# Kernel optimization log

Measured on AMD Instinct MI355X. Metric: run time of the kernel, lower is better.

The kernel has to match this reference:

```python
import jax, jax.numpy as jnp
import numpy as np

H = 1024
W = 1024
N = 128
K1 = 21.7  # on-road exponential loss scale
K2 = 40.0  # off-road exponential loss scale


def setup_inputs() -> dict:
    key = jax.random.key(0)
    k1, k2 = jax.random.split(key)
    hd_map = (jax.random.uniform(k1, (H, W)) < 0.3).astype(jnp.float32)
    # integer pixel coordinates, kept away from the border so the 2x2
    # neighbor window is always in-bounds (matches typical usage)
    prediction = jax.random.randint(k2, (N, 2), 2, H - 2).astype(jnp.int32)
    return {"hd_map": hd_map, "prediction": prediction}


def reference(hd_map, prediction):
    Hm, Wm = hd_map.shape
    p = prediction.astype(jnp.float32)  # [N,2]

    # Separable squared distances from each point to every pixel.
    # NOTE: faithful to the original, nonzero()[:,0] (row) is compared with
    # point[0] and nonzero()[:,1] (col) with point[1].
    rows = jnp.arange(Hm, dtype=jnp.float32)
    cols = jnp.arange(Wm, dtype=jnp.float32)
    dr2 = (rows[None, :] - p[:, 0:1]) ** 2  # [N,H]
    dc2 = (cols[None, :] - p[:, 1:2]) ** 2  # [N,W]
    d2 = dr2[:, :, None] + dc2[:, None, :]  # [N,H,W]

    INF = jnp.float32(1e30)
    on_mask = hd_map != 0  # nonzero pixels of hd_map (non-drivable)
    # min squared distance to nearest nonzero pixel of hd_map
    d2_on = jnp.min(jnp.where(on_mask[None], d2, INF), axis=(1, 2))  # [N]
    # min squared distance to nearest nonzero pixel of (1 - hd_map)
    d2_off = jnp.min(jnp.where(on_mask[None], INF, d2), axis=(1, 2))  # [N]

    px = prediction[:, 0]
    py = prediction[:, 1]
    # is_outside_frame: point[0] vs shape[0], point[1] vs shape[1] (faithful)
    outside_frame = (px < 0) | (px > Hm) | (py < 0) | (py > Wm)

    # is_outside_road: 2x2 window im[py-1:py+1, px-1:px+1] contains a 1
    ir = jnp.stack([py - 1, py - 1, py, py], axis=-1)  # [N,4]
    ic = jnp.stack([px - 1, px, px - 1, px], axis=-1)  # [N,4]
    neigh = hd_map[ir, ic]  # [N,4]
    outside_road = jnp.any(neigh == 1.0, axis=-1)

    ln2 = jnp.log(jnp.float32(2.0))
    # off-road: exp(d * ln(2)/k2); on-road: exp(-d^2 / k1)
    loss_off = jnp.exp(jnp.sqrt(d2_off) * (ln2 / K2))
    loss_on = jnp.exp(-d2_on / K1)

    per_point = jnp.where(
        outside_frame,
        jnp.float32(0.0),
        jnp.where(outside_road, loss_off, loss_on),
    )
    return jnp.mean(per_point)
```

## Files before the change

kernel.cpp:

```cpp
#include <hip/hip_runtime.h>
#include <math.h>

#define HMAP 1024
#define WMAP 1024

__device__ __forceinline__ int clampi(int x, int hi) {
    return x < 0 ? 0 : (x > hi ? hi : x);
}

__global__ __launch_bounds__(64)
void roadloss_points(const float* __restrict__ hd_map,
                     const int* __restrict__ pred,
                     int n,
                     float* __restrict__ ws) {
    const int pt   = blockIdx.x;
    const int lane = threadIdx.x;
    if (pt >= n) return;

    const int px = pred[2 * pt];
    const int py = pred[2 * pt + 1];

    const int r0c = clampi(py - 1, HMAP - 1), r1c = clampi(py, HMAP - 1);
    const int c0c = clampi(px - 1, WMAP - 1), c1c = clampi(px, WMAP - 1);
    const float n00 = hd_map[r0c * WMAP + c0c];
    const float n01 = hd_map[r0c * WMAP + c1c];
    const float n10 = hd_map[r1c * WMAP + c0c];
    const float n11 = hd_map[r1c * WMAP + c1c];

    const int R = 16;

    float v[18];
#pragma unroll
    for (int ii = 0; ii < 18; ++ii) {
        int i  = lane + ii * 64;
        int dr = i / 33 - R;
        int dc = i % 33 - R;
        int r  = clampi(px + dr, HMAP - 1);
        int c  = clampi(py + dc, WMAP - 1);
        v[ii]  = hd_map[r * WMAP + c];
    }

    float on0 = 1e30f, off0 = 1e30f, on1 = 1e30f, off1 = 1e30f;
#pragma unroll
    for (int ii = 0; ii < 18; ++ii) {
        int i  = lane + ii * 64;
        int dr = i / 33 - R;
        int dc = i % 33 - R;
        bool inb = (i < 33 * 33) &&
                   ((unsigned)(px + dr) < (unsigned)HMAP) &&
                   ((unsigned)(py + dc) < (unsigned)WMAP);
        float d2 = (float)(dr * dr + dc * dc);
        if (inb) {
            if (ii & 1) {
                if (v[ii] != 0.0f) on1  = fminf(on1,  d2);
                else               off1 = fminf(off1, d2);
            } else {
                if (v[ii] != 0.0f) on0  = fminf(on0,  d2);
                else               off0 = fminf(off0, d2);
            }
        }
    }
    float best_on  = fminf(on0,  on1);
    float best_off = fminf(off0, off1);

#pragma unroll
    for (int s = 1; s < 64; s <<= 1) {
        best_on  = fminf(best_on,  __shfl_xor(best_on,  s, 64));
        best_off = fminf(best_off, __shfl_xor(best_off, s, 64));
    }

    const float guard = (float)((R + 1) * (R + 1));
    if (!(best_on <= guard && best_off <= guard)) {
        for (int i = lane; i < HMAP * WMAP; i += 64) {
            int r = i >> 10, c = i & (WMAP - 1);
            int dri = r - px, dci = c - py;
            float d2 = (float)(dri * dri + dci * dci);
            float m = hd_map[i];
            if (m != 0.0f) best_on  = fminf(best_on,  d2);
            else           best_off = fminf(best_off, d2);
        }
#pragma unroll
        for (int s = 1; s < 64; s <<= 1) {
            best_on  = fminf(best_on,  __shfl_xor(best_on,  s, 64));
            best_off = fminf(best_off, __shfl_xor(best_off, s, 64));
        }
    }

    if (lane == 0) {
        bool outside_frame = (px < 0) | (px > HMAP) | (py < 0) | (py > WMAP);
        bool outside_road  = (n00 == 1.0f) | (n01 == 1.0f) |
                             (n10 == 1.0f) | (n11 == 1.0f);
        const float K1 = 21.7f, K2 = 40.0f;
        const float LN2 = 0.6931471805599453f;
        ws[pt] = outside_frame
                     ? 0.0f
                     : (outside_road ? expf(sqrtf(best_off) * (LN2 / K2))
                                     : expf(-best_on / K1));
    }
}

__global__ __launch_bounds__(64)
void roadloss_reduce(const float* __restrict__ ws, int n,
                     float* __restrict__ out) {
    const int lane = threadIdx.x;
    float s = 0.0f;
    for (int i = lane; i < n; i += 64) s += ws[i];
#pragma unroll
    for (int d = 1; d < 64; d <<= 1) s += __shfl_xor(s, d, 64);
    if (lane == 0) out[0] = s / (float)n;
}

extern "C" void kernel_launch(void* const* d_in, const int* in_sizes, int n_in,
                              void* d_out, int out_size, void* d_ws, size_t ws_size,
                              hipStream_t stream) {
    const float* hd_map = (const float*)d_in[0];
    const int*   pred   = (const int*)d_in[1];
    float* out = (float*)d_out;
    float* ws  = (float*)d_ws;
    int n = in_sizes[1] / 2;

    roadloss_points<<<n, 64, 0, stream>>>(hd_map, pred, n, ws);
    roadloss_reduce<<<1, 64, 0, stream>>>(ws, n, out);
}
```

Before: 58.29 us.

## Fuse per-point search and mean into one block with smaller windows

Replaces the two-kernel scheme (one 64-thread block per point, then a reduce) with a single 1024-thread block. Each block handles several points, one per 16-lane group of a wavefront. The local search window shrinks from 33x33 to 11x11, and the full-map fallback runs only for points the small window cannot settle. The mean is reduced in shared memory, which removes a launch and the workspace round trip. In exchange, the fallback is more likely to fire with the small window, and it is serialized per wave, so all work now runs on one CU.

```diff
diff --git a/kernel.cpp b/kernel.cpp
--- a/kernel.cpp
+++ b/kernel.cpp
@@ -3,122 +3,148 @@
 
 #define HMAP 1024
 #define WMAP 1024
+#define NW 16
 
 __device__ __forceinline__ int clampi(int x, int hi) {
     return x < 0 ? 0 : (x > hi ? hi : x);
 }
 
-__global__ __launch_bounds__(64)
-void roadloss_points(const float* __restrict__ hd_map,
-                     const int* __restrict__ pred,
-                     int n,
-                     float* __restrict__ ws) {
-    const int pt   = blockIdx.x;
-    const int lane = threadIdx.x;
-    if (pt >= n) return;
+__global__ __launch_bounds__(1024)
+void roadloss_fused(const float* __restrict__ hd_map,
+                    const int* __restrict__ pred,
+                    int n,
+                    float* __restrict__ out) {
+    __shared__ float lds_loss[1024];
 
-    const int px = pred[2 * pt];
-    const int py = pred[2 * pt + 1];
+    const int tid  = threadIdx.x;
+    const int w    = tid >> 6;
+    const int lane = tid & 63;
+    const int g    = lane >> 4;
+    const int t    = lane & 15;
 
-    const int r0c = clampi(py - 1, HMAP - 1), r1c = clampi(py, HMAP - 1);
-    const int c0c = clampi(px - 1, WMAP - 1), c1c = clampi(px, WMAP - 1);
-    const float n00 = hd_map[r0c * WMAP + c0c];
-    const float n01 = hd_map[r0c * WMAP + c1c];
-    const float n10 = hd_map[r1c * WMAP + c0c];
-    const float n11 = hd_map[r1c * WMAP + c1c];
+    const int   R     = 5;
+    const float GUARD = 36.0f;
 
-    const int R = 16;
+    const int nslots = (n + NW - 1) / NW;
 
-    float v[18];
+    for (int sb = 0; sb < nslots; sb += 4) {
+        const int  s     = sb + g;
+        const int  pt    = w + NW * s;
+        const bool valid = (s < nslots) && (pt < n);
+        const int  ptc   = valid ? pt : 0;
+
+        const int2 pp = ((const int2*)pred)[ptc];
+        const int  px = pp.x;
+        const int  py = pp.y;
+
+        float pv[8];
+        float d2v[8];
+        bool  inb[8];
 #pragma unroll
-    for (int ii = 0; ii < 18; ++ii) {
-        int i  = lane + ii * 64;
-        int dr = i / 33 - R;
-        int dc = i % 33 - R;
-        int r  = clampi(px + dr, HMAP - 1);
-        int c  = clampi(py + dc, WMAP - 1);
-        v[ii]  = hd_map[r * WMAP + c];
-    }
+        for (int ii = 0; ii < 8; ++ii) {
+            int i   = t + 16 * ii;
+            int dr  = i / 11 - R;
+            int dc  = i % 11 - R;
+            int r   = clampi(px + dr, HMAP - 1);
+            int c   = clampi(py + dc, WMAP - 1);
+            pv[ii]  = hd_map[r * WMAP + c];
+            d2v[ii] = (float)(dr * dr + dc * dc);
+            inb[ii] = (i < 121) &&
+                      ((unsigned)(px + dr) < (unsigned)HMAP) &&
+                      ((unsigned)(py + dc) < (unsigned)WMAP);
+        }
 
-    float on0 = 1e30f, off0 = 1e30f, on1 = 1e30f, off1 = 1e30f;
+        float nv = 0.0f;
+        if (t < 4) {
+            int r = clampi(py - 1 + (t >> 1), HMAP - 1);
+            int c = clampi(px - 1 + (t & 1), WMAP - 1);
+            nv = hd_map[r * WMAP + c];
+        }
+        const unsigned long long road_mask = __ballot(nv == 1.0f);
+        const bool outside_road = ((road_mask >> (g * 16)) & 0xFull) != 0ull;
+
+        float on0 = 1e30f, off0 = 1e30f, on1 = 1e30f, off1 = 1e30f;
 #pragma unroll
-    for (int ii = 0; ii < 18; ++ii) {
-        int i  = lane + ii * 64;
-        int dr = i / 33 - R;
-        int dc = i % 33 - R;
-        bool inb = (i < 33 * 33) &&
-                   ((unsigned)(px + dr) < (unsigned)HMAP) &&
-                   ((unsigned)(py + dc) < (unsigned)WMAP);
-        float d2 = (float)(dr * dr + dc * dc);
-        if (inb) {
-            if (ii & 1) {
-                if (v[ii] != 0.0f) on1  = fminf(on1,  d2);
-                else               off1 = fminf(off1, d2);
-            } else {
-                if (v[ii] != 0.0f) on0  = fminf(on0,  d2);
-                else               off0 = fminf(off0, d2);
+        for (int ii = 0; ii < 8; ++ii) {
+            if (inb[ii]) {
+                if (ii & 1) {
+                    if (pv[ii] != 0.0f) on1  = fminf(on1,  d2v[ii]);
+                    else                off1 = fminf(off1, d2v[ii]);
+                } else {
+                    if (pv[ii] != 0.0f) on0  = fminf(on0,  d2v[ii]);
+                    else                off0 = fminf(off0, d2v[ii]);
+                }
             }
         }
-    }
-    float best_on  = fminf(on0,  on1);
-    float best_off = fminf(off0, off1);
+        float best_on  = fminf(on0, on1);
+        float best_off = fminf(off0, off1);
+#pragma unroll
+        for (int sh = 1; sh < 16; sh <<= 1) {
+            best_on  = fminf(best_on,  __shfl_xor(best_on,  sh, 64));
+            best_off = fminf(best_off, __shfl_xor(best_off, sh, 64));
+        }
 
+        unsigned long long fmask =
+            __ballot(valid && (t == 0) &&
+                     !(best_on <= GUARD && best_off <= GUARD));
+        if (__builtin_expect(fmask != 0ull, 0)) {
+            while (fmask) {
+                int src = __ffsll((long long)fmask) - 1;
+                fmask &= fmask - 1;
+                int   fpx = __shfl(px, src, 64);
+                int   fpy = __shfl(py, src, 64);
+                float bo  = __shfl(best_on,  src, 64);
+                float bf  = __shfl(best_off, src, 64);
+                for (int i = lane; i < HMAP * WMAP; i += 64) {
+                    int r = i >> 10, c = i & (WMAP - 1);
+                    int dri = r - fpx, dci = c - fpy;
+                    float d2 = (float)(dri * dri + dci * dci);
+                    float m  = hd_map[i];
+                    if (m != 0.0f) bo = fminf(bo, d2);
+                    else           bf = fminf(bf, d2);
+                }
 #pragma unroll
-    for (int s = 1; s < 64; s <<= 1) {
-        best_on  = fminf(best_on,  __shfl_xor(best_on,  s, 64));
-        best_off = fminf(best_off, __shfl_xor(best_off, s, 64));
-    }
+                for (int sh = 1; sh < 64; sh <<= 1) {
+                    bo = fminf(bo, __shfl_xor(bo, sh, 64));
+                    bf = fminf(bf, __shfl_xor(bf, sh, 64));
+                }
+                if ((lane >> 4) == (src >> 4)) {
+                    best_on  = bo;
+                    best_off = bf;
+                }
+            }
+        }
 
-    const float guard = (float)((R + 1) * (R + 1));
-    if (!(best_on <= guard && best_off <= guard)) {
-        for (int i = lane; i < HMAP * WMAP; i += 64) {
-            int r = i >> 10, c = i & (WMAP - 1);
-            int dri = r - px, dci = c - py;
-            float d2 = (float)(dri * dri + dci * dci);
-            float m = hd_map[i];
-            if (m != 0.0f) best_on  = fminf(best_on,  d2);
-            else           best_off = fminf(best_off, d2);
-        }
-#pragma unroll
-        for (int s = 1; s < 64; s <<= 1) {
-            best_on  = fminf(best_on,  __shfl_xor(best_on,  s, 64));
-            best_off = fminf(best_off, __shfl_xor(best_off, s, 64));
+        if (valid && (t == 0) && pt < 1024) {
+            bool outside_frame =
+                (px < 0) | (px > HMAP) | (py < 0) | (py > WMAP);
+            const float K1  = 21.7f, K2 = 40.0f;
+            const float LN2 = 0.6931471805599453f;
+            lds_loss[pt] = outside_frame
+                ? 0.0f
+                : (outside_road ? expf(sqrtf(best_off) * (LN2 / K2))
+                                : expf(-best_on / K1));
         }
     }
 
-    if (lane == 0) {
-        bool outside_frame = (px < 0) | (px > HMAP) | (py < 0) | (py > WMAP);
-        bool outside_road  = (n00 == 1.0f) | (n01 == 1.0f) |
-                             (n10 == 1.0f) | (n11 == 1.0f);
-        const float K1 = 21.7f, K2 = 40.0f;
-        const float LN2 = 0.6931471805599453f;
-        ws[pt] = outside_frame
-                     ? 0.0f
-                     : (outside_road ? expf(sqrtf(best_off) * (LN2 / K2))
-                                     : expf(-best_on / K1));
+    __syncthreads();
+
+    if (w == 0) {
+        float sum = 0.0f;
+        for (int i = lane; i < n; i += 64) sum += lds_loss[i];
+#pragma unroll
+        for (int d = 1; d < 64; d <<= 1) sum += __shfl_xor(sum, d, 64);
+        if (lane == 0) out[0] = sum / (float)n;
     }
 }
 
-__global__ __launch_bounds__(64)
-void roadloss_reduce(const float* __restrict__ ws, int n,
-                     float* __restrict__ out) {
-    const int lane = threadIdx.x;
-    float s = 0.0f;
-    for (int i = lane; i < n; i += 64) s += ws[i];
-#pragma unroll
-    for (int d = 1; d < 64; d <<= 1) s += __shfl_xor(s, d, 64);
-    if (lane == 0) out[0] = s / (float)n;
-}
-
 extern "C" void kernel_launch(void* const* d_in, const int* in_sizes, int n_in,
-                              void* d_out, int out_size, void* d_ws, size_t ws_size,
-                              hipStream_t stream) {
+                              void* d_out, int out_size, void* d_ws,
+                              size_t ws_size, hipStream_t stream) {
     const float* hd_map = (const float*)d_in[0];
     const int*   pred   = (const int*)d_in[1];
     float* out = (float*)d_out;
-    float* ws  = (float*)d_ws;
     int n = in_sizes[1] / 2;
 
-    roadloss_points<<<n, 64, 0, stream>>>(hd_map, pred, n, ws);
-    roadloss_reduce<<<1, 64, 0, stream>>>(ws, n, out);
+    roadloss_fused<<<1, 1024, 0, stream>>>(hd_map, pred, n, out);
 }
```

Measured after the change: 59.88 us. 2.7% more time.
